# Kernel optimization log

Measured on AMD Instinct MI355X. Metric: run time of the kernel, lower is better.

## Reference

```python
import jax, jax.numpy as jnp
import numpy as np

# Assumptions (SubNetwork / SelfAttention source not provided):
#  - SubNetwork(in_dim, hidden, 3) is a VectorNet polyline subgraph: 3 layers of
#    (Linear->ReLU) followed by maxpool-over-nodes concat, so per-node dim -> 2*hidden.
#    Layer in-dims: in_dim, 2h, 2h; the graph argument is structural and unused in the math.
#  - SelfAttention(D, D) is single-head scaled dot-product self-attention returning
#    (output, attn_weights); the [0] in forward selects the output.
#  - map_mask is all ones, so max_mask == M and every map polyline is processed.

def _nan0(x):
    return jnp.where(jnp.isnan(x), jnp.zeros_like(x), x)

def _subnet(x, Ws, Bs):
    # x: [G, T, N, in] -> per-graph global feature [G, T, 2h]
    for W, b in zip(Ws, Bs):
        h = jax.nn.relu(x @ W + b)                       # [G,T,N,h]
        agg = jnp.max(h, axis=2, keepdims=True)           # [G,T,1,h]
        x = jnp.concatenate([h, jnp.broadcast_to(agg, h.shape)], axis=-1)
    return jnp.max(x, axis=2)                             # [G,T,2h]


def setup_inputs() -> dict:
    key = jax.random.key(0)
    ks = jax.random.split(key, 32)
    in_dim, h, D, out_dim = 16, 64, 128, 60
    A, M, O, T, Na, Nm, No = 4, 64, 32, 32, 256, 256, 128

    def w(k, shape, fan_in):
        return jax.random.normal(k, shape, dtype=jnp.float32) / np.sqrt(fan_in).astype(np.float32)

    inp = {
        'agent_set': jnp.zeros((A, 1), jnp.float32),
        'map_set': jnp.zeros((M, 1), jnp.float32),
        'agent_feature': jax.random.normal(ks[0], (A, T, Na, in_dim), dtype=jnp.float32),
        'map_feature': jax.random.normal(ks[1], (M, T, Nm, in_dim), dtype=jnp.float32),
        'map_mask': jnp.ones((T, M), jnp.int32),
        'obj_set': jnp.zeros((O, 1), jnp.float32),
        'obj_feature': jax.random.normal(ks[2], (O, T, No, in_dim), dtype=jnp.float32),
    }
    # subnetwork params (agent / map / obj)
    names = ['a', 'm', 'o']
    for i, n in enumerate(names):
        base = 3 + i * 3
        inp[n + 'W0'] = w(ks[base + 0], (in_dim, h), in_dim)
        inp[n + 'B0'] = jnp.zeros((h,), jnp.float32)
        inp[n + 'W1'] = w(ks[base + 1], (2 * h, h), 2 * h)
        inp[n + 'B1'] = jnp.zeros((h,), jnp.float32)
        inp[n + 'W2'] = w(ks[base + 2], (2 * h, h), 2 * h)
        inp[n + 'B2'] = jnp.zeros((h,), jnp.float32)
    inp['Wq'] = w(ks[12], (D, D), D)
    inp['Wk'] = w(ks[13], (D, D), D)
    inp['Wv'] = w(ks[14], (D, D), D)
    inp['mlpW1'] = w(ks[15], (A, D, D), D)
    inp['mlpB1'] = jnp.zeros((A, D), jnp.float32)
    inp['mlpW2'] = w(ks[16], (A, D, out_dim), D)
    inp['mlpB2'] = jnp.zeros((A, out_dim), jnp.float32)
    return inp


def reference(agent_set, map_set, agent_feature, map_feature, map_mask, obj_set, obj_feature,
              aW0, aB0, aW1, aB1, aW2, aB2,
              mW0, mB0, mW1, mB1, mW2, mB2,
              oW0, oB0, oW1, oB1, oW2, oB2,
              Wq, Wk, Wv, mlpW1, mlpB1, mlpW2, mlpB2):
    af = _nan0(agent_feature)
    ag = _subnet(af, (aW0, aW1, aW2), (aB0, aB1, aB2))    # [A,T,D]
    # original only NaN-masks the first agent's global feature
    ag = jnp.concatenate([_nan0(ag[:1]), ag[1:]], axis=0)
    # map_mask rows all sum to M -> max_mask == M, use all map polylines
    mg = _subnet(map_feature, (mW0, mW1, mW2), (mB0, mB1, mB2))  # [M,T,D]
    og = _subnet(obj_feature, (oW0, oW1, oW2), (oB0, oB1, oB2))  # [O,T,D]
    G = jnp.concatenate([ag, mg, og], axis=0)              # [E,T,D]
    x = jnp.transpose(G, (1, 0, 2))                        # [T,E,D]
    q, k, v = x @ Wq, x @ Wk, x @ Wv
    scale = np.float32(1.0 / np.sqrt(x.shape[-1]))
    attn = jax.nn.softmax(jnp.einsum('ted,tfd->tef', q, k) * scale, axis=-1)
    o = jnp.einsum('tef,tfd->ted', attn, v)                # [T,E,D]
    hdn = jnp.tanh(jnp.einsum('ted,adh->ateh', o, mlpW1) + mlpB1[:, None, None, :])
    out = jnp.einsum('ateh,aho->ateo', hdn, mlpW2) + mlpB2[:, None, None, :]
    return out  # [num_agents=4, T, E, out_dim]
```

## Files before the change

kernel.cpp:

```cpp
#include <hip/hip_runtime.h>
#include <hip/hip_fp16.h>

#define TT 32
#define EN 100
#define DD 128

typedef _Float16 half4 __attribute__((ext_vector_type(4)));
typedef _Float16 half2v __attribute__((ext_vector_type(2)));
typedef float f32x4 __attribute__((ext_vector_type(4)));

#define MFMA16(a, b, c) __builtin_amdgcn_mfma_f32_16x16x16f16((a), (b), (c), 0, 0, 0)

__device__ __forceinline__ float nan0f(float v) { return (v == v) ? v : 0.f; }

__device__ __forceinline__ float ftanh(float x) {
    x = fminf(9.f, fmaxf(-9.f, x));
    float e = __expf(2.f * x);
    return (e - 1.f) / (e + 1.f);
}

__device__ __forceinline__ half2v pk2(float lo, float hi) {
    auto v = __builtin_amdgcn_cvt_pkrtz(lo, hi);
    half2v r;
    __builtin_memcpy(&r, &v, 4);
    return r;
}

__device__ __forceinline__ int ldsoff(int ps, int row, int col) {
    int b = (col >> 6) * ps + row * 136 + ((col & 63) << 1);
    return b ^ ((row & 12) << 2);
}

__device__ __forceinline__ int hoff(int row, int col) {
    return (row * 136 + (col << 1)) ^ ((row & 12) << 2);
}

#define OFF_AW   0
#define OFF_MW   2304
#define OFF_OW   4608
#define OFF_QKV  6912
#define OFF_MW1  19200
#define OFF_MW2  35584

struct PackArgs {
    const float* src[20];
    int C[20], VC[20], ktc[20], ntc[20], dsto[20], ar[20];
};

__global__ __launch_bounds__(256) void pack_w(PackArgs pa, _Float16* __restrict__ dst)
{
    const int s = blockIdx.y;
    const int total = pa.ktc[s] * pa.ntc[s] * 64;
    const int i = blockIdx.x * 256 + threadIdx.x;
    if (i >= total) return;
    const int ml = i & 15, gq = (i >> 4) & 3, rest = i >> 6;
    const int ntc = pa.ntc[s];
    const int nt = rest % ntc, kt = rest / ntc;
    const int col = nt * 16 + ml, row0 = kt * 16 + gq * 4;
    const float* W = pa.src[s];
    const int C = pa.C[s], VC = pa.VC[s], ar = pa.ar[s];
    half4 v;
#pragma unroll
    for (int j = 0; j < 4; ++j) {
        float fv = 0.f;
        if (col < VC) {
            fv = W[(size_t)(row0 + j) * C + col];
            if (ar) fv += W[(size_t)(row0 + j + ar) * C + col];
        }
        v[j] = (_Float16)fv;
    }
    *(half4*)(dst + ((size_t)pa.dsto[s] + i) * 4) = v;
}

struct SubArgs {
    const float* feat[3];
    const _Float16* wp[3];
    const float* B0[3];
    const float* W1[3]; const float* B1[3];
    const float* W2[3]; const float* B2[3];
    int e_base[3];
    int lo[3];
    int dn[3];
};

__global__ __launch_bounds__(512, 4) void subnet_uber(SubArgs sa, _Float16* __restrict__ xh)
{
    const int bid = blockIdx.x;
    const int s = (bid >= sa.lo[1]) + (bid >= sa.lo[2]);
    const int tid = threadIdx.x;
    const int w = tid >> 6, lane = tid & 63, ml = lane & 15, gq = lane >> 4;
    const bool hm = (s == 2);
    const int h = hm ? (w >> 2) : 0;
    const int wl = hm ? (w & 3) : w;
    const int idx = hm ? ((bid - sa.lo[2]) * 2 + h) : (bid - sa.lo[s]);
    const int g = idx >> 5, t = idx & 31;
    const int N = hm ? 128 : 256;
    const int rowL = wl * 32;
    const int hsb = h * 128;
    const int grp0 = h * 4;

    __shared__ __attribute__((aligned(16))) unsigned char Hs[256 * 136];
    __shared__ float red[8][64];
    __shared__ float part[8][64];

    f32x4 acc[2][4];
    float cvr[4];

    auto epilogue = [&](bool store) {
#pragma unroll
        for (int nt = 0; nt < 4; ++nt) {
            float am;
            if (store) {
                const half2v zz = {(_Float16)0.f, (_Float16)0.f};
                half2v amh = zz;
#pragma unroll
                for (int mt = 0; mt < 2; ++mt) {
                    f32x4 v = acc[mt][nt];
                    half2v p0 = __builtin_elementwise_max(pk2(v.x, v.y), zz);
                    half2v p1 = __builtin_elementwise_max(pk2(v.z, v.w), zz);
                    amh = __builtin_elementwise_max(
                        amh, __builtin_elementwise_max(p0, p1));
                    const int r0 = hsb + rowL + mt * 16 + gq * 4;
                    const int c = nt * 16 + ml;
                    unsigned u0, u1;
                    __builtin_memcpy(&u0, &p0, 4);
                    __builtin_memcpy(&u1, &p1, 4);
                    *(unsigned short*)(Hs + hoff(r0 + 0, c)) = (unsigned short)u0;
                    *(unsigned short*)(Hs + hoff(r0 + 1, c)) = (unsigned short)(u0 >> 16);
                    *(unsigned short*)(Hs + hoff(r0 + 2, c)) = (unsigned short)u1;
                    *(unsigned short*)(Hs + hoff(r0 + 3, c)) = (unsigned short)(u1 >> 16);
                }
                am = fmaxf((float)amh[0], (float)amh[1]);
            } else {
                am = 0.f;
#pragma unroll
                for (int mt = 0; mt < 2; ++mt) {
                    f32x4 v = acc[mt][nt];
                    am = fmaxf(am, fmaxf(fmaxf(v.x, v.y), fmaxf(v.z, v.w)));
                }
            }
            am = fmaxf(am, __shfl_xor(am, 16, 64));
            am = fmaxf(am, __shfl_xor(am, 32, 64));
            if (lane < 16) red[w][nt * 16 + lane] = am;
        }
        __syncthreads();
    };

    auto group_max = [&]() {
        float a = red[grp0][lane];
#pragma unroll
        for (int ww = 1; ww < 4; ++ww) a = fmaxf(a, red[grp0 + ww][lane]);
        if (!hm) {
#pragma unroll
            for (int ww = 4; ww < 8; ++ww) a = fmaxf(a, red[ww][lane]);
        }
        return a;
    };

    auto make_cvec = [&](const float* Wn, const float* Bn) {
        float a = group_max();
        float sum = 0.f;
        if (hm) {
#pragma unroll
            for (int kk = 0; kk < 16; ++kk) {
                int k = wl * 16 + kk;
                sum = fmaf(__shfl(a, k, 64), Wn[(size_t)(64 + k) * 64 + lane], sum);
            }
        } else {
#pragma unroll
            for (int kk = 0; kk < 8; ++kk) {
                int k = w * 8 + kk;
                sum = fmaf(__shfl(a, k, 64), Wn[(size_t)(64 + k) * 64 + lane], sum);
            }
        }
        part[w][lane] = sum;
        __syncthreads();
        float c = Bn[lane];
#pragma unroll
        for (int ww = 0; ww < 4; ++ww) c += part[grp0 + ww][lane];
        if (!hm) {
#pragma unroll
            for (int ww = 4; ww < 8; ++ww) c += part[ww][lane];
        }
#pragma unroll
        for (int nt = 0; nt < 4; ++nt) cvr[nt] = __shfl(c, nt * 16 + ml, 64);
    };

    const _Float16* wp = sa.wp[s];

    {
        const float* B0 = sa.B0[s];
#pragma unroll
        for (int nt = 0; nt < 4; ++nt) {
            float b = B0[nt * 16 + ml];
            acc[0][nt] = f32x4{b, b, b, b};
            acc[1][nt] = f32x4{b, b, b, b};
        }
        half4 bf[4];
#pragma unroll
        for (int nt = 0; nt < 4; ++nt)
            bf[nt] = *(const half4*)(wp + (size_t)(((nt * 4 + gq) * 16 + ml) * 4));
        const float* xb = sa.feat[s] + (size_t)idx * N * 16;
        const int dn = sa.dn[s];
#pragma unroll
        for (int mt = 0; mt < 2; ++mt) {
            float4 xv = *reinterpret_cast<const float4*>(
                xb + (size_t)(rowL + mt * 16 + ml) * 16 + gq * 4);
            if (dn) {
                xv.x = nan0f(xv.x); xv.y = nan0f(xv.y);
                xv.z = nan0f(xv.z); xv.w = nan0f(xv.w);
            }
            half4 af = half4{(_Float16)xv.x, (_Float16)xv.y,
                             (_Float16)xv.z, (_Float16)xv.w};
#pragma unroll
            for (int nt = 0; nt < 4; ++nt)
                acc[mt][nt] = MFMA16(af, bf[nt], acc[mt][nt]);
        }
    }
    epilogue(true);
    make_cvec(sa.W1[s], sa.B1[s]);

    auto layer = [&](const _Float16* wb, bool store) {
#pragma unroll
        for (int nt = 0; nt < 4; ++nt) {
            float cv = cvr[nt];
            acc[0][nt] = f32x4{cv, cv, cv, cv};
            acc[1][nt] = f32x4{cv, cv, cv, cv};
        }
#pragma unroll
        for (int kt = 0; kt < 4; ++kt) {
            half4 bf[4];
#pragma unroll
            for (int nt = 0; nt < 4; ++nt)
                bf[nt] = *(const half4*)(wb +
                    (size_t)(((((kt * 4 + nt) * 4) + gq) * 16 + ml) * 4));
#pragma unroll
            for (int mt = 0; mt < 2; ++mt) {
                half4 af = *(const half4*)(Hs +
                    hoff(hsb + rowL + mt * 16 + ml, kt * 16 + gq * 4));
#pragma unroll
                for (int nt = 0; nt < 4; ++nt)
                    acc[mt][nt] = MFMA16(af, bf[nt], acc[mt][nt]);
            }
        }
        epilogue(store);
    };

    layer(wp + 256 * 4, true);
    make_cvec(sa.W2[s], sa.B2[s]);
    layer(wp + 1280 * 4, false);

    if (wl == 0) {
        float a = group_max();
        size_t base = ((size_t)t * 112 + (sa.e_base[s] + g)) * 64;
        xh[base + lane] = (_Float16)a;
    }
}

#define PSX 15232
#define WSO 30464

__global__ __launch_bounds__(256) void qkv_kernel(
    const _Float16* __restrict__ xh, const _Float16* __restrict__ wqkv,
    _Float16* __restrict__ qh, _Float16* __restrict__ kh, _Float16* __restrict__ vh)
{
    const int t = blockIdx.x;
    const int tgt = blockIdx.y;
    const int tid = threadIdx.x;
    const int w = tid >> 6, lane = tid & 63, ml = lane & 15, gq = lane >> 4;

    const _Float16* wb = wqkv + (size_t)tgt * 2048 * 4;
    _Float16* Oh = (tgt == 0) ? qh : (tgt == 1) ? kh : vh;

#pragma unroll 1
    for (int mi = 0; mi < 2; ++mi) {
        int mt = w + (mi << 2);
        if (mt >= 7) continue;
        const int srow = min(mt * 16 + ml, EN - 1);
        half4 xa[4];
#pragma unroll
        for (int kt = 0; kt < 4; ++kt)
            xa[kt] = *(const half4*)(xh + (size_t)t * 7168 + srow * 64 + kt * 16 + gq * 4);
#pragma unroll
        for (int nt = 0; nt < 8; ++nt) {
            f32x4 acc = {0.f, 0.f, 0.f, 0.f};
#pragma unroll
            for (int kt = 0; kt < 4; ++kt) {
                half4 b = *(const half4*)(wb +
                    (size_t)(((((kt * 8 + nt) * 4) + gq) * 16 + ml) * 4));
                acc = MFMA16(xa[kt], b, acc);
            }
            _Float16* op = Oh + (size_t)t * 14336 + (mt * 16 + gq * 4) * 128 + nt * 16 + ml;
            op[0]   = (_Float16)acc.x;
            op[128] = (_Float16)acc.y;
            op[256] = (_Float16)acc.z;
            op[384] = (_Float16)acc.w;
        }
    }
}

#define VSO 30464

__global__ __launch_bounds__(256) void attn_kernel(
    const _Float16* __restrict__ qh, const _Float16* __restrict__ kh,
    const _Float16* __restrict__ vh, _Float16* __restrict__ obufh)
{
    const int t = blockIdx.x;
    const int rb = blockIdx.y;
    const int tid = threadIdx.x;
    const int w = tid >> 6, lane = tid & 63, ml = lane & 15, gq = lane >> 4;

    __shared__ __attribute__((aligned(16))) unsigned char sm[2 * WSO];

    const int mt = rb * 2 + w;
    const bool act = (w < 2) && (mt < 7);

    half4 qa[8];
    if (act) {
#pragma unroll
        for (int kt = 0; kt < 8; ++kt)
            qa[kt] = *(const half4*)(qh + (size_t)t * 14336 + (mt * 16 + ml) * 128
                                     + kt * 16 + gq * 4);
    }

    for (int i = tid; i < 112 * 32; i += 256) {
        int row = i >> 5, c4 = (i & 31) << 2;
        size_t src = (size_t)t * 14336 + row * 128 + c4;
        *(half4*)(sm + ldsoff(PSX, row, c4))       = *(const half4*)(kh + src);
        *(half4*)(sm + VSO + ldsoff(PSX, row, c4)) = *(const half4*)(vh + src);
    }
    __syncthreads();

    const float scale = 0.088388347648318447f;
    half4 pf[7];

    if (act) {
        f32x4 sacc[7];
#pragma unroll
        for (int nt = 0; nt < 7; ++nt) {
            f32x4 acc = {0.f, 0.f, 0.f, 0.f};
#pragma unroll
            for (int kt = 0; kt < 8; ++kt) {
                half4 b = *(const half4*)(sm + ldsoff(PSX, nt * 16 + ml, kt * 16 + gq * 4));
                acc = MFMA16(qa[kt], b, acc);
            }
            sacc[nt].x = acc.x * scale; sacc[nt].y = acc.y * scale;
            sacc[nt].z = acc.z * scale; sacc[nt].w = acc.w * scale;
        }
        float mx[4] = {-3e38f, -3e38f, -3e38f, -3e38f};
#pragma unroll
        for (int nt = 0; nt < 7; ++nt) {
            if (nt < 6 || ml < 4) {
                mx[0] = fmaxf(mx[0], sacc[nt].x); mx[1] = fmaxf(mx[1], sacc[nt].y);
                mx[2] = fmaxf(mx[2], sacc[nt].z); mx[3] = fmaxf(mx[3], sacc[nt].w);
            }
        }
#pragma unroll
        for (int m = 1; m <= 8; m <<= 1) {
#pragma unroll
            for (int i = 0; i < 4; ++i) mx[i] = fmaxf(mx[i], __shfl_xor(mx[i], m, 64));
        }
        float sum[4] = {0.f, 0.f, 0.f, 0.f};
#pragma unroll
        for (int nt = 0; nt < 7; ++nt) {
            bool v = (nt < 6) || (ml < 4);
            float p0 = v ? __expf(sacc[nt].x - mx[0]) : 0.f;
            float p1 = v ? __expf(sacc[nt].y - mx[1]) : 0.f;
            float p2 = v ? __expf(sacc[nt].z - mx[2]) : 0.f;
            float p3 = v ? __expf(sacc[nt].w - mx[3]) : 0.f;
            sum[0] += p0; sum[1] += p1; sum[2] += p2; sum[3] += p3;
            sacc[nt] = f32x4{p0, p1, p2, p3};
        }
#pragma unroll
        for (int m = 1; m <= 8; m <<= 1) {
#pragma unroll
            for (int i = 0; i < 4; ++i) sum[i] += __shfl_xor(sum[i], m, 64);
        }
        float inv[4] = {1.f / sum[0], 1.f / sum[1], 1.f / sum[2], 1.f / sum[3]};
#pragma unroll
        for (int nt = 0; nt < 7; ++nt)
            pf[nt] = half4{(_Float16)(sacc[nt].x * inv[0]), (_Float16)(sacc[nt].y * inv[1]),
                           (_Float16)(sacc[nt].z * inv[2]), (_Float16)(sacc[nt].w * inv[3])};
    }

    __syncthreads();

    if (act) {
        const int row0 = mt * 16 + gq * 4;
#pragma unroll
        for (int nt = 0; nt < 7; ++nt) {
            const int col = nt * 16 + ml;
            *(_Float16*)(sm + ldsoff(PSX, row0 + 0, col)) = pf[nt].x;
            *(_Float16*)(sm + ldsoff(PSX, row0 + 1, col)) = pf[nt].y;
            *(_Float16*)(sm + ldsoff(PSX, row0 + 2, col)) = pf[nt].z;
            *(_Float16*)(sm + ldsoff(PSX, row0 + 3, col)) = pf[nt].w;
        }

        half4 pa[7];
#pragma unroll
        for (int kt = 0; kt < 7; ++kt)
            pa[kt] = *(const half4*)(sm + ldsoff(PSX, mt * 16 + ml, kt * 16 + gq * 4));
#pragma unroll
        for (int nt = 0; nt < 8; ++nt) {
            f32x4 acc = {0.f, 0.f, 0.f, 0.f};
            const int col = nt * 16 + ml;
#pragma unroll
            for (int kt = 0; kt < 7; ++kt) {
                const int r0 = kt * 16 + gq * 4;
                half4 b = half4{
                    *(const _Float16*)(sm + VSO + ldsoff(PSX, r0 + 0, col)),
                    *(const _Float16*)(sm + VSO + ldsoff(PSX, r0 + 1, col)),
                    *(const _Float16*)(sm + VSO + ldsoff(PSX, r0 + 2, col)),
                    *(const _Float16*)(sm + VSO + ldsoff(PSX, r0 + 3, col))};
                acc = MFMA16(pa[kt], b, acc);
            }
            const int row0 = mt * 16 + gq * 4;
            _Float16* op = obufh + (size_t)t * EN * DD + row0 * DD + col;
            if (row0 + 0 < EN) op[0]       = (_Float16)acc.x;
            if (row0 + 1 < EN) op[DD]      = (_Float16)acc.y;
            if (row0 + 2 < EN) op[2 * DD]  = (_Float16)acc.z;
            if (row0 + 3 < EN) op[3 * DD]  = (_Float16)acc.w;
        }
    }
}

#define PSH 8704

__global__ __launch_bounds__(256) void mlp_kernel(
    const _Float16* __restrict__ obufh, const _Float16* __restrict__ wpk,
    const float* __restrict__ B1, const float* __restrict__ B2,
    float* __restrict__ out)
{
    const int a = blockIdx.y;
    const int tid = threadIdx.x;
    const int w = tid >> 6, lane = tid & 63, ml = lane & 15, gq = lane >> 4;
    const int rowbase = blockIdx.x * 64 + w * 16;

    __shared__ __attribute__((aligned(16))) unsigned char sm[PSH * 2];

    const _Float16* w1b = wpk + ((size_t)OFF_MW1 + a * 4096) * 4;
    const _Float16* w2b = wpk + ((size_t)OFF_MW2 + a * 2048) * 4;

    half4 xa[8];
#pragma unroll
    for (int kt = 0; kt < 8; ++kt)
        xa[kt] = *(const half4*)(obufh + (size_t)(rowbase + ml) * 128
                                 + kt * 16 + gq * 4);
#pragma unroll
    for (int nt = 0; nt < 8; ++nt) {
        const int col = nt * 16 + ml;
        float bv = B1[a * 128 + col];
        f32x4 acc = {bv, bv, bv, bv};
#pragma unroll
        for (int kt = 0; kt < 8; ++kt) {
            half4 b = *(const half4*)(w1b +
                (size_t)(((((kt * 8 + nt) * 4) + gq) * 16 + ml) * 4));
            acc = MFMA16(xa[kt], b, acc);
        }
        const int lr0 = w * 16 + gq * 4;
        *(_Float16*)(sm + ldsoff(PSH, lr0 + 0, col)) = (_Float16)ftanh(acc.x);
        *(_Float16*)(sm + ldsoff(PSH, lr0 + 1, col)) = (_Float16)ftanh(acc.y);
        *(_Float16*)(sm + ldsoff(PSH, lr0 + 2, col)) = (_Float16)ftanh(acc.z);
        *(_Float16*)(sm + ldsoff(PSH, lr0 + 3, col)) = (_Float16)ftanh(acc.w);
    }

    half4 ha[8];
#pragma unroll
    for (int kt = 0; kt < 8; ++kt)
        ha[kt] = *(const half4*)(sm + ldsoff(PSH, w * 16 + ml, kt * 16 + gq * 4));
#pragma unroll
    for (int nt = 0; nt < 4; ++nt) {
        const int o = nt * 16 + ml;
        const bool valid = o < 60;
        float bv = valid ? B2[a * 60 + o] : 0.f;
        f32x4 acc = {bv, bv, bv, bv};
#pragma unroll
        for (int kt = 0; kt < 8; ++kt) {
            half4 b = *(const half4*)(w2b +
                (size_t)(((((kt * 4 + nt) * 4) + gq) * 16 + ml) * 4));
            acc = MFMA16(ha[kt], b, acc);
        }
        if (valid) {
            float* op = out + (size_t)a * 192000 + (size_t)(rowbase + gq * 4) * 60 + o;
            op[0]   = acc.x;
            op[60]  = acc.y;
            op[120] = acc.z;
            op[180] = acc.w;
        }
    }
}

extern "C" void kernel_launch(void* const* d_in, const int* in_sizes, int n_in,
                              void* d_out, int out_size, void* d_ws, size_t ws_size,
                              hipStream_t stream)
{
    const float* agent_feature = (const float*)d_in[2];
    const float* map_feature   = (const float*)d_in[3];
    const float* obj_feature   = (const float*)d_in[6];
    const float* aW0 = (const float*)d_in[7];  const float* aB0 = (const float*)d_in[8];
    const float* aW1 = (const float*)d_in[9];  const float* aB1 = (const float*)d_in[10];
    const float* aW2 = (const float*)d_in[11]; const float* aB2 = (const float*)d_in[12];
    const float* mW0 = (const float*)d_in[13]; const float* mB0 = (const float*)d_in[14];
    const float* mW1 = (const float*)d_in[15]; const float* mB1 = (const float*)d_in[16];
    const float* mW2 = (const float*)d_in[17]; const float* mB2 = (const float*)d_in[18];
    const float* oW0 = (const float*)d_in[19]; const float* oB0 = (const float*)d_in[20];
    const float* oW1 = (const float*)d_in[21]; const float* oB1 = (const float*)d_in[22];
    const float* oW2 = (const float*)d_in[23]; const float* oB2 = (const float*)d_in[24];
    const float* Wq = (const float*)d_in[25];
    const float* Wk = (const float*)d_in[26];
    const float* Wv = (const float*)d_in[27];
    const float* mlpW1 = (const float*)d_in[28]; const float* mlpB1 = (const float*)d_in[29];
    const float* mlpW2 = (const float*)d_in[30]; const float* mlpB2 = (const float*)d_in[31];

    _Float16* xh    = (_Float16*)d_ws;
    _Float16* qh    = xh + 229376;
    _Float16* kh    = qh + 458752;
    _Float16* vh    = kh + 458752;
    _Float16* obufh = vh + 458752;
    _Float16* wpk   = obufh + 409600;

    float* outp = (float*)d_out;

    PackArgs pa;
    auto seg = [&](int s, const float* src, int C, int VC, int ktc, int ntc,
                   int dsto, int ar = 0) {
        pa.src[s] = src; pa.C[s] = C; pa.VC[s] = VC;
        pa.ktc[s] = ktc; pa.ntc[s] = ntc; pa.dsto[s] = dsto; pa.ar[s] = ar;
    };
    seg(0, aW0, 64, 64, 1, 4, OFF_AW);
    seg(1, aW1, 64, 64, 4, 4, OFF_AW + 256);
    seg(2, aW2, 64, 64, 4, 4, OFF_AW + 1280);
    seg(3, mW0, 64, 64, 1, 4, OFF_MW);
    seg(4, mW1, 64, 64, 4, 4, OFF_MW + 256);
    seg(5, mW2, 64, 64, 4, 4, OFF_MW + 1280);
    seg(6, oW0, 64, 64, 1, 4, OFF_OW);
    seg(7, oW1, 64, 64, 4, 4, OFF_OW + 256);
    seg(8, oW2, 64, 64, 4, 4, OFF_OW + 1280);
    seg(9,  Wq, 128, 128, 4, 8, OFF_QKV,        64);
    seg(10, Wk, 128, 128, 4, 8, OFF_QKV + 2048, 64);
    seg(11, Wv, 128, 128, 4, 8, OFF_QKV + 4096, 64);
    for (int a = 0; a < 4; ++a) {
        seg(12 + a, mlpW1 + (size_t)a * 16384, 128, 128, 8, 8, OFF_MW1 + a * 4096);
        seg(16 + a, mlpW2 + (size_t)a * 7680,  60,  60,  8, 4, OFF_MW2 + a * 2048);
    }
    pack_w<<<dim3(16, 20), 256, 0, stream>>>(pa, wpk);

    SubArgs sa;
    sa.feat[0] = agent_feature; sa.feat[1] = map_feature; sa.feat[2] = obj_feature;
    sa.wp[0] = wpk + OFF_AW * 4; sa.wp[1] = wpk + OFF_MW * 4; sa.wp[2] = wpk + OFF_OW * 4;
    sa.B0[0] = aB0; sa.B0[1] = mB0; sa.B0[2] = oB0;
    sa.W1[0] = aW1; sa.W1[1] = mW1; sa.W1[2] = oW1;
    sa.B1[0] = aB1; sa.B1[1] = mB1; sa.B1[2] = oB1;
    sa.W2[0] = aW2; sa.W2[1] = mW2; sa.W2[2] = oW2;
    sa.B2[0] = aB2; sa.B2[1] = mB2; sa.B2[2] = oB2;
    sa.e_base[0] = 0; sa.e_base[1] = 4; sa.e_base[2] = 68;
    sa.lo[0] = 0; sa.lo[1] = 128; sa.lo[2] = 128 + 2048;
    sa.dn[0] = 1; sa.dn[1] = 0; sa.dn[2] = 0;
    subnet_uber<<<dim3(2688), 512, 0, stream>>>(sa, xh);

    qkv_kernel<<<dim3(TT, 3), 256, 0, stream>>>(xh, wpk + OFF_QKV * 4, qh, kh, vh);
    attn_kernel<<<dim3(TT, 4), 256, 0, stream>>>(qh, kh, vh, obufh);
    mlp_kernel<<<dim3(50, 4), 256, 0, stream>>>(obufh, wpk, mlpB1, mlpB2, outp);
}
```

Measured before the change: 84.44 us.

## Fold Wq·Wkᵀ into a 64x64 matrix and drop the K projection

```diff
diff --git a/kernel.cpp b/kernel.cpp
--- a/kernel.cpp
+++ b/kernel.cpp
@@ -70,6 +70,23 @@
         v[j] = (_Float16)fv;
     }
     *(half4*)(dst + ((size_t)pa.dsto[s] + i) * 4) = v;
+}
+
+__global__ __launch_bounds__(256) void pack_m(
+    const float* __restrict__ Wq, const float* __restrict__ Wk,
+    _Float16* __restrict__ dst)
+{
+    const int i = blockIdx.x * 256 + threadIdx.x;
+    const int a = i >> 6, b = i & 63;
+    float s = 0.f;
+    for (int c = 0; c < 128; ++c) {
+        float q  = Wq[(size_t)a * 128 + c] + Wq[(size_t)(a + 64) * 128 + c];
+        float kk = Wk[(size_t)b * 128 + c] + Wk[(size_t)(b + 64) * 128 + c];
+        s = fmaf(q, kk, s);
+    }
+    const int kt = a >> 4, gq = (a >> 2) & 3, j = a & 3;
+    const int nt = b >> 4, ml = b & 15;
+    dst[(size_t)(((((kt * 4 + nt) * 4) + gq) * 16 + ml) * 4) + j] = (_Float16)s;
 }
 
 struct SubArgs {
@@ -258,19 +275,15 @@
 }
 
 #define PSX 15232
-#define WSO 30464
-
-__global__ __launch_bounds__(256) void qkv_kernel(
+
+__global__ __launch_bounds__(256) void qv_kernel(
     const _Float16* __restrict__ xh, const _Float16* __restrict__ wqkv,
-    _Float16* __restrict__ qh, _Float16* __restrict__ kh, _Float16* __restrict__ vh)
+    _Float16* __restrict__ qh, _Float16* __restrict__ vh)
 {
     const int t = blockIdx.x;
     const int tgt = blockIdx.y;
     const int tid = threadIdx.x;
     const int w = tid >> 6, lane = tid & 63, ml = lane & 15, gq = lane >> 4;
-
-    const _Float16* wb = wqkv + (size_t)tgt * 2048 * 4;
-    _Float16* Oh = (tgt == 0) ? qh : (tgt == 1) ? kh : vh;
 
 #pragma unroll 1
     for (int mi = 0; mi < 2; ++mi) {
@@ -281,28 +294,50 @@
 #pragma unroll
         for (int kt = 0; kt < 4; ++kt)
             xa[kt] = *(const half4*)(xh + (size_t)t * 7168 + srow * 64 + kt * 16 + gq * 4);
-#pragma unroll
-        for (int nt = 0; nt < 8; ++nt) {
-            f32x4 acc = {0.f, 0.f, 0.f, 0.f};
-#pragma unroll
-            for (int kt = 0; kt < 4; ++kt) {
-                half4 b = *(const half4*)(wb +
-                    (size_t)(((((kt * 8 + nt) * 4) + gq) * 16 + ml) * 4));
-                acc = MFMA16(xa[kt], b, acc);
-            }
-            _Float16* op = Oh + (size_t)t * 14336 + (mt * 16 + gq * 4) * 128 + nt * 16 + ml;
-            op[0]   = (_Float16)acc.x;
-            op[128] = (_Float16)acc.y;
-            op[256] = (_Float16)acc.z;
-            op[384] = (_Float16)acc.w;
-        }
-    }
-}
-
-#define VSO 30464
+        if (tgt == 0) {
+            const _Float16* wb = wqkv;
+#pragma unroll
+            for (int nt = 0; nt < 4; ++nt) {
+                f32x4 acc = {0.f, 0.f, 0.f, 0.f};
+#pragma unroll
+                for (int kt = 0; kt < 4; ++kt) {
+                    half4 b = *(const half4*)(wb +
+                        (size_t)(((((kt * 4 + nt) * 4) + gq) * 16 + ml) * 4));
+                    acc = MFMA16(xa[kt], b, acc);
+                }
+                _Float16* op = qh + (size_t)t * 7168 + (mt * 16 + gq * 4) * 64 + nt * 16 + ml;
+                op[0]   = (_Float16)acc.x;
+                op[64]  = (_Float16)acc.y;
+                op[128] = (_Float16)acc.z;
+                op[192] = (_Float16)acc.w;
+            }
+        } else {
+            const _Float16* wb = wqkv + 1024 * 4;
+#pragma unroll
+            for (int nt = 0; nt < 8; ++nt) {
+                f32x4 acc = {0.f, 0.f, 0.f, 0.f};
+#pragma unroll
+                for (int kt = 0; kt < 4; ++kt) {
+                    half4 b = *(const half4*)(wb +
+                        (size_t)(((((kt * 8 + nt) * 4) + gq) * 16 + ml) * 4));
+                    acc = MFMA16(xa[kt], b, acc);
+                }
+                _Float16* op = vh + (size_t)t * 14336 + (mt * 16 + gq * 4) * 128 + nt * 16 + ml;
+                op[0]   = (_Float16)acc.x;
+                op[128] = (_Float16)acc.y;
+                op[256] = (_Float16)acc.z;
+                op[384] = (_Float16)acc.w;
+            }
+        }
+    }
+}
+
+#define XSO 0
+#define VVO 15232
+#define PPO 45696
 
 __global__ __launch_bounds__(256) void attn_kernel(
-    const _Float16* __restrict__ qh, const _Float16* __restrict__ kh,
+    const _Float16* __restrict__ qh, const _Float16* __restrict__ xh,
     const _Float16* __restrict__ vh, _Float16* __restrict__ obufh)
 {
     const int t = blockIdx.x;
@@ -310,29 +345,32 @@
     const int tid = threadIdx.x;
     const int w = tid >> 6, lane = tid & 63, ml = lane & 15, gq = lane >> 4;
 
-    __shared__ __attribute__((aligned(16))) unsigned char sm[2 * WSO];
+    __shared__ __attribute__((aligned(16))) unsigned char sm[76160];
 
     const int mt = rb * 2 + w;
     const bool act = (w < 2) && (mt < 7);
 
-    half4 qa[8];
+    half4 qa[4];
     if (act) {
 #pragma unroll
-        for (int kt = 0; kt < 8; ++kt)
-            qa[kt] = *(const half4*)(qh + (size_t)t * 14336 + (mt * 16 + ml) * 128
+        for (int kt = 0; kt < 4; ++kt)
+            qa[kt] = *(const half4*)(qh + (size_t)t * 7168 + (mt * 16 + ml) * 64
                                      + kt * 16 + gq * 4);
     }
 
+    for (int i = tid; i < 112 * 16; i += 256) {
+        int row = i >> 4, c4 = (i & 15) << 2;
+        *(half4*)(sm + XSO + ldsoff(PSX, row, c4)) =
+            *(const half4*)(xh + (size_t)t * 7168 + row * 64 + c4);
+    }
     for (int i = tid; i < 112 * 32; i += 256) {
         int row = i >> 5, c4 = (i & 31) << 2;
-        size_t src = (size_t)t * 14336 + row * 128 + c4;
-        *(half4*)(sm + ldsoff(PSX, row, c4))       = *(const half4*)(kh + src);
-        *(half4*)(sm + VSO + ldsoff(PSX, row, c4)) = *(const half4*)(vh + src);
+        *(half4*)(sm + VVO + ldsoff(PSX, row, c4)) =
+            *(const half4*)(vh + (size_t)t * 14336 + row * 128 + c4);
     }
     __syncthreads();
 
     const float scale = 0.088388347648318447f;
-    half4 pf[7];
 
     if (act) {
         f32x4 sacc[7];
@@ -340,8 +378,9 @@
         for (int nt = 0; nt < 7; ++nt) {
             f32x4 acc = {0.f, 0.f, 0.f, 0.f};
 #pragma unroll
-            for (int kt = 0; kt < 8; ++kt) {
-                half4 b = *(const half4*)(sm + ldsoff(PSX, nt * 16 + ml, kt * 16 + gq * 4));
+            for (int kt = 0; kt < 4; ++kt) {
+                half4 b = *(const half4*)(sm + XSO +
+                    ldsoff(PSX, nt * 16 + ml, kt * 16 + gq * 4));
                 acc = MFMA16(qa[kt], b, acc);
             }
             sacc[nt].x = acc.x * scale; sacc[nt].y = acc.y * scale;
@@ -377,29 +416,26 @@
             for (int i = 0; i < 4; ++i) sum[i] += __shfl_xor(sum[i], m, 64);
         }
         float inv[4] = {1.f / sum[0], 1.f / sum[1], 1.f / sum[2], 1.f / sum[3]};
-#pragma unroll
-        for (int nt = 0; nt < 7; ++nt)
-            pf[nt] = half4{(_Float16)(sacc[nt].x * inv[0]), (_Float16)(sacc[nt].y * inv[1]),
-                           (_Float16)(sacc[nt].z * inv[2]), (_Float16)(sacc[nt].w * inv[3])};
-    }
-
-    __syncthreads();
-
-    if (act) {
+
         const int row0 = mt * 16 + gq * 4;
 #pragma unroll
         for (int nt = 0; nt < 7; ++nt) {
             const int col = nt * 16 + ml;
-            *(_Float16*)(sm + ldsoff(PSX, row0 + 0, col)) = pf[nt].x;
-            *(_Float16*)(sm + ldsoff(PSX, row0 + 1, col)) = pf[nt].y;
-            *(_Float16*)(sm + ldsoff(PSX, row0 + 2, col)) = pf[nt].z;
-            *(_Float16*)(sm + ldsoff(PSX, row0 + 3, col)) = pf[nt].w;
+            *(_Float16*)(sm + PPO + ldsoff(PSX, row0 + 0, col)) =
+                (_Float16)(sacc[nt].x * inv[0]);
+            *(_Float16*)(sm + PPO + ldsoff(PSX, row0 + 1, col)) =
+                (_Float16)(sacc[nt].y * inv[1]);
+            *(_Float16*)(sm + PPO + ldsoff(PSX, row0 + 2, col)) =
+                (_Float16)(sacc[nt].z * inv[2]);
+            *(_Float16*)(sm + PPO + ldsoff(PSX, row0 + 3, col)) =
+                (_Float16)(sacc[nt].w * inv[3]);
         }
 
         half4 pa[7];
 #pragma unroll
         for (int kt = 0; kt < 7; ++kt)
-            pa[kt] = *(const half4*)(sm + ldsoff(PSX, mt * 16 + ml, kt * 16 + gq * 4));
+            pa[kt] = *(const half4*)(sm + PPO +
+                ldsoff(PSX, mt * 16 + ml, kt * 16 + gq * 4));
 #pragma unroll
         for (int nt = 0; nt < 8; ++nt) {
             f32x4 acc = {0.f, 0.f, 0.f, 0.f};
@@ -408,13 +444,12 @@
             for (int kt = 0; kt < 7; ++kt) {
                 const int r0 = kt * 16 + gq * 4;
                 half4 b = half4{
-                    *(const _Float16*)(sm + VSO + ldsoff(PSX, r0 + 0, col)),
-                    *(const _Float16*)(sm + VSO + ldsoff(PSX, r0 + 1, col)),
-                    *(const _Float16*)(sm + VSO + ldsoff(PSX, r0 + 2, col)),
-                    *(const _Float16*)(sm + VSO + ldsoff(PSX, r0 + 3, col))};
+                    *(const _Float16*)(sm + VVO + ldsoff(PSX, r0 + 0, col)),
+                    *(const _Float16*)(sm + VVO + ldsoff(PSX, r0 + 1, col)),
+                    *(const _Float16*)(sm + VVO + ldsoff(PSX, r0 + 2, col)),
+                    *(const _Float16*)(sm + VVO + ldsoff(PSX, r0 + 3, col))};
                 acc = MFMA16(pa[kt], b, acc);
             }
-            const int row0 = mt * 16 + gq * 4;
             _Float16* op = obufh + (size_t)t * EN * DD + row0 * DD + col;
             if (row0 + 0 < EN) op[0]       = (_Float16)acc.x;
             if (row0 + 1 < EN) op[DD]      = (_Float16)acc.y;
@@ -514,8 +549,7 @@
 
     _Float16* xh    = (_Float16*)d_ws;
     _Float16* qh    = xh + 229376;
-    _Float16* kh    = qh + 458752;
-    _Float16* vh    = kh + 458752;
+    _Float16* vh    = qh + 229376;
     _Float16* obufh = vh + 458752;
     _Float16* wpk   = obufh + 409600;
 
@@ -536,14 +570,13 @@
     seg(6, oW0, 64, 64, 1, 4, OFF_OW);
     seg(7, oW1, 64, 64, 4, 4, OFF_OW + 256);
     seg(8, oW2, 64, 64, 4, 4, OFF_OW + 1280);
-    seg(9,  Wq, 128, 128, 4, 8, OFF_QKV,        64);
-    seg(10, Wk, 128, 128, 4, 8, OFF_QKV + 2048, 64);
-    seg(11, Wv, 128, 128, 4, 8, OFF_QKV + 4096, 64);
+    seg(9, Wv, 128, 128, 4, 8, OFF_QKV + 1024, 64);
     for (int a = 0; a < 4; ++a) {
-        seg(12 + a, mlpW1 + (size_t)a * 16384, 128, 128, 8, 8, OFF_MW1 + a * 4096);
-        seg(16 + a, mlpW2 + (size_t)a * 7680,  60,  60,  8, 4, OFF_MW2 + a * 2048);
-    }
-    pack_w<<<dim3(16, 20), 256, 0, stream>>>(pa, wpk);
+        seg(10 + a, mlpW1 + (size_t)a * 16384, 128, 128, 8, 8, OFF_MW1 + a * 4096);
+        seg(14 + a, mlpW2 + (size_t)a * 7680,  60,  60,  8, 4, OFF_MW2 + a * 2048);
+    }
+    pack_w<<<dim3(16, 18), 256, 0, stream>>>(pa, wpk);
+    pack_m<<<dim3(16), 256, 0, stream>>>(Wq, Wk, wpk + OFF_QKV * 4);
 
     SubArgs sa;
     sa.feat[0] = agent_feature; sa.feat[1] = map_feature; sa.feat[2] = obj_feature;
@@ -558,7 +591,7 @@
     sa.dn[0] = 1; sa.dn[1] = 0; sa.dn[2] = 0;
     subnet_uber<<<dim3(2688), 512, 0, stream>>>(sa, xh);
 
-    qkv_kernel<<<dim3(TT, 3), 256, 0, stream>>>(xh, wpk + OFF_QKV * 4, qh, kh, vh);
-    attn_kernel<<<dim3(TT, 4), 256, 0, stream>>>(qh, kh, vh, obufh);
+    qv_kernel<<<dim3(TT, 2), 256, 0, stream>>>(xh, wpk + OFF_QKV * 4, qh, vh);
+    attn_kernel<<<dim3(TT, 4), 256, 0, stream>>>(qh, xh, vh, obufh);
     mlp_kernel<<<dim3(50, 4), 256, 0, stream>>>(obufh, wpk, mlpB1, mlpB2, outp);
 }
```

Measured after the change: 102.3 us. +21.2%, slower.
